# Kernel optimization log

Measured on AMD Instinct MI355X. Metric: run time of the kernel, lower is better.

## Reference

```python
import jax, jax.numpy as jnp
import numpy as np

EPS = 1e-6

def setup_inputs() -> dict:
    key = jax.random.key(0)
    M, N, D = 6, 4096, 512
    output = jax.random.normal(key, (M, N, D), dtype=jnp.float32)
    return {"output": output}

def reference(output):
    # output: [M, N, D] stacked per-layer features (already flatten(1)'d)
    M, N, _ = output.shape
    # Gram matrices K_i = X_i @ X_i^T with zeroed diagonal: [M, N, N]
    K = jnp.einsum('ind,imd->inm', output, output)
    K = K * (1.0 - jnp.eye(N, dtype=K.dtype))
    # Double centering H@K@H == K - rowmean - colmean + totalmean
    row = jnp.mean(K, axis=2, keepdims=True)
    col = jnp.mean(K, axis=1, keepdims=True)
    tot = jnp.mean(K, axis=(1, 2), keepdims=True)
    Khat = K - row - col + tot
    # Pairwise HSIC(K_i, K_j) = |sum(Khat_i * Khat_j)| : [M, M]
    S = jnp.abs(jnp.einsum('inm,jnm->ij', Khat, Khat))
    diag = jnp.diagonal(S)
    cka = S / jnp.sqrt(diag[:, None] * diag[None, :] + EPS)
    # Original only fills the strict lower triangle
    hsic_matrix = cka * jnp.tril(jnp.ones((M, M), dtype=cka.dtype), k=-1)
    l = jnp.sum(jnp.abs(hsic_matrix))
    hsic_visual = hsic_matrix + hsic_matrix.T + jnp.eye(M, dtype=cka.dtype)
    return (hsic_visual, l)
```

## Files before the change

### kernel.cpp

```cpp
#include <hip/hip_runtime.h>
#include <hip/hip_bf16.h>
#include <stdint.h>


#define NPTS  4096
#define DF    512
#define ML    6
#define NPAIR 21
#define BKB   128
#define KCHUNK_O 512
#define KCHUNK_D 1024
#define NDIAGBLK 240
#define NOFFBLK  960
#define NGEMMBLK (NDIAGBLK + NOFFBLK)

typedef float  f32x4 __attribute__((ext_vector_type(4)));
typedef unsigned char u8;
typedef long long i64;

__constant__ int c_PI[NPAIR] = {0,0,0,0,0,0, 1,1,1,1,1, 2,2,2,2, 3,3,3, 4,4, 5};
__constant__ int c_PJ[NPAIR] = {0,1,2,3,4,5, 1,2,3,4,5, 2,3,4,5, 3,4,5, 4,5, 5};
__constant__ int c_DIAGP[ML]  = {0, 6, 11, 15, 18, 20};
__constant__ int c_OFFP[15]   = {1,2,3,4,5, 7,8,9,10, 12,13,14, 16,17, 19};
__constant__ int c_TM[10] = {0,0,0,0, 1,1,1, 2,2, 3};
__constant__ int c_TN[10] = {0,1,2,3, 1,2,3, 2,3, 3};

#define OFF_XT8 0u
#define OFF_CP  12582912u
#define OFF_S   (OFF_CP + 15728640u)
#define OFF_F   (OFF_S + 12288u)
#define OFF_D   (OFF_F + 512u)
#define OFF_XS  (OFF_D + 98304u)
#define ZERO_BYTES (12288u + 512u + 98304u + 98304u)
#define OFF_DD  (OFF_XS + 98304u)
#define OFF_RD  (OFF_DD + 256u)
#define OFF_T   (OFF_RD + 256u)

__device__ __forceinline__ unsigned short f2fp8x2(float a, float b) {
    return (unsigned short)(__builtin_amdgcn_cvt_pk_fp8_f32(a, b, 0, false) & 0xffff);
}

__device__ __forceinline__ void gl2lds16(const void* g, void* l) {
    __builtin_amdgcn_global_load_lds(
        (__attribute__((address_space(1))) void*)g,
        (__attribute__((address_space(3))) void*)l, 16, 0, 0);
}

__global__ __launch_bounds__(256) void k_transpose(const float* __restrict__ X,
                                                   u8* __restrict__ Xt8,
                                                   float* __restrict__ s,
                                                   float* __restrict__ dv) {
    __shared__ float tT[64][67];
    int l = blockIdx.z, n0 = blockIdx.x * 64, d0 = blockIdx.y * 64;
    int t = threadIdx.x, q = t & 15, r = t >> 4;
    const float4* src = (const float4*)(X + ((size_t)l * NPTS + n0) * DF + d0);
#pragma unroll
    for (int p = 0; p < 4; ++p) {
        int rr = r + 16 * p;
        float4 v = src[(size_t)rr * (DF / 4) + q];
        tT[4 * q + 0][rr] = v.x;
        tT[4 * q + 1][rr] = v.y;
        tT[4 * q + 2][rr] = v.z;
        tT[4 * q + 3][rr] = v.w;
    }
    __syncthreads();
    if (t < 64) {
        float cs = 0.f;
#pragma unroll
        for (int k = 0; k < 64; ++k) {
            int n = (6 * t + k) & 63;
            cs += tT[t][n];
        }
        atomicAdd(&s[l * DF + d0 + t], cs);
    } else if (t < 128) {
        int n = t - 64;
        float rs = 0.f;
#pragma unroll
        for (int d = 0; d < 64; ++d) { float v = tT[d][n]; rs += v * v; }
        atomicAdd(&dv[l * NPTS + n0 + n], rs);
    }
    int dcol = t >> 2, nb = (t & 3) * 16;
    uint4 o;
#pragma unroll
    for (int w2 = 0; w2 < 4; ++w2) {
        int j = nb + w2 * 4;
        unsigned lo = f2fp8x2(tT[dcol][j + 0], tT[dcol][j + 1]);
        unsigned hi = f2fp8x2(tT[dcol][j + 2], tT[dcol][j + 3]);
        ((unsigned*)&o)[w2] = lo | (hi << 16);
    }
    *(uint4*)(Xt8 + ((size_t)(l * DF + d0 + dcol)) * NPTS + n0 + nb) = o;
}

__global__ __launch_bounds__(256) void k_rowdot(const u8* __restrict__ Xt8,
                                                const float* __restrict__ s,
                                                float* __restrict__ xs) {
    int l = blockIdx.z, d0 = blockIdx.y * 64, n0 = blockIdx.x * 1024;
    int t = threadIdx.x;
    __shared__ float sl[64];
    if (t < 64) sl[t] = s[l * DF + d0 + t];
    __syncthreads();
    const u8* base = Xt8 + ((size_t)(l * DF + d0)) * NPTS + n0 + t * 4;
    float a0 = 0, a1 = 0, a2 = 0, a3 = 0;
#pragma unroll 8
    for (int d = 0; d < 64; ++d) {
        unsigned v = *(const unsigned*)(base + (size_t)d * NPTS);
        float sv = sl[d];
        a0 += sv * __builtin_amdgcn_cvt_f32_fp8(v, 0);
        a1 += sv * __builtin_amdgcn_cvt_f32_fp8(v, 1);
        a2 += sv * __builtin_amdgcn_cvt_f32_fp8(v, 2);
        a3 += sv * __builtin_amdgcn_cvt_f32_fp8(v, 3);
    }
    float* o = xs + l * NPTS + n0 + t * 4;
    atomicAdd(&o[0], a0); atomicAdd(&o[1], a1);
    atomicAdd(&o[2], a2); atomicAdd(&o[3], a3);
}

__global__ __launch_bounds__(256) void k_pairdots(const float* __restrict__ dv,
                                                  const float* __restrict__ xs,
                                                  const float* __restrict__ s,
                                                  float* __restrict__ ddot,
                                                  float* __restrict__ rdot,
                                                  float* __restrict__ tb) {
    int p = blockIdx.x, i = c_PI[p], j = c_PJ[p];
    int t = threadIdx.x;
    const float invN = 1.0f / (float)NPTS;
    float dd = 0.f, rr = 0.f, sd = 0.f, ss = 0.f;
    for (int n = t; n < NPTS; n += 256) {
        float di = dv[i * NPTS + n], dj = dv[j * NPTS + n];
        float ri = (xs[i * NPTS + n] - di) * invN;
        float rj = (xs[j * NPTS + n] - dj) * invN;
        dd += di * dj;
        rr += ri * rj;
        sd += di;
    }
    for (int c = t; c < DF; c += 256) { float v = s[i * DF + c]; ss += v * v; }
    __shared__ float4 red[256];
    red[t] = make_float4(dd, rr, sd, ss);
    __syncthreads();
    for (int h = 128; h > 0; h >>= 1) {
        if (t < h) {
            float4 a = red[t], b = red[t + h];
            red[t] = make_float4(a.x + b.x, a.y + b.y, a.z + b.z, a.w + b.w);
        }
        __syncthreads();
    }
    if (t == 0) {
        ddot[p] = red[0].x;
        rdot[p] = red[0].y;
        if (i == j)
            tb[i] = (red[0].w - red[0].z) * (1.0f / ((float)NPTS * (float)NPTS));
    }
}

__global__ __launch_bounds__(256, 2) void k_gemm_frob(const u8* __restrict__ Xt8,
                                                      float* __restrict__ CP,
                                                      float* __restrict__ F) {
    __shared__ __align__(16) u8 As[128 * BKB];
    __shared__ __align__(16) u8 Bs[256 * BKB];

    int b = blockIdx.x;
    int t = threadIdx.x, wave = t >> 6, lane = t & 63;
    int rl = lane >> 3, g = lane & 7;
    int row16 = lane & 15, quad = lane >> 4;
    int qh = quad >> 1, qb = (quad & 1) * 8;

    if (b < NDIAGBLK) {
        int li = b / 40, rem = b % 40, tt = rem >> 2, z = rem & 3;
        int mt = c_TM[tt], nt = c_TN[tt];
        const u8* A = Xt8 + ((size_t)(li * DF + mt * 128)) * NPTS;
        const u8* B = Xt8 + ((size_t)(li * DF + nt * 128)) * NPTS;
        int kLo = z * KCHUNK_D, kHi = kLo + KCHUNK_D;

        int wr = (wave >> 1) * 64, wc = (wave & 1) * 64;
        f32x4 acc[4][4];
#pragma unroll
        for (int mi = 0; mi < 4; ++mi)
#pragma unroll
            for (int ni = 0; ni < 4; ++ni) acc[mi][ni] = (f32x4)0.0f;

        for (int k0 = kLo; k0 < kHi; k0 += BKB) {
            __syncthreads();
#pragma unroll
            for (int is = 0; is < 4; ++is) {
                int rbase = is * 32 + wave * 8;
                int r = rbase + rl;
                int gs = g ^ (r & 7);
                gl2lds16(A + (size_t)r * NPTS + k0 + gs * 16, &As[rbase * BKB]);
                gl2lds16(B + (size_t)r * NPTS + k0 + gs * 16, &Bs[rbase * BKB]);
            }
            __syncthreads();
#pragma unroll
            for (int ko = 0; ko < 4; ++ko) {
                int gi = ko * 2 + qh;
                i64 af[4], bf[4];
#pragma unroll
                for (int mi = 0; mi < 4; ++mi) {
                    int row = wr + mi * 16 + row16;
                    af[mi] = *(const i64*)&As[row * BKB + (gi ^ (row & 7)) * 16 + qb];
                }
#pragma unroll
                for (int ni = 0; ni < 4; ++ni) {
                    int row = wc + ni * 16 + row16;
                    bf[ni] = *(const i64*)&Bs[row * BKB + (gi ^ (row & 7)) * 16 + qb];
                }
#pragma unroll
                for (int mi = 0; mi < 4; ++mi)
#pragma unroll
                    for (int ni = 0; ni < 4; ++ni)
                        acc[mi][ni] = __builtin_amdgcn_mfma_f32_16x16x32_fp8_fp8(
                            af[mi], bf[ni], acc[mi][ni], 0, 0, 0);
            }
        }
        float* cp = CP + (((size_t)(li * 10 + tt) * 4 + z) * 16384) + wave * 4096;
#pragma unroll
        for (int mi = 0; mi < 4; ++mi)
#pragma unroll
            for (int ni = 0; ni < 4; ++ni)
#pragma unroll
                for (int e = 0; e < 4; ++e)
                    cp[(mi * 4 + ni) * 256 + e * 64 + lane] = acc[mi][ni][e];
    } else {
        int b2 = b - NDIAGBLK;
        int op = b2 >> 6, rem = b2 & 63;
        int tile = rem >> 3, z = rem & 7;
        int pp = c_OFFP[op];
        const u8* A = Xt8 + ((size_t)(c_PI[pp] * DF + (tile & 3) * 128)) * NPTS;
        const u8* B = Xt8 + ((size_t)(c_PJ[pp] * DF + (tile >> 2) * 256)) * NPTS;
        int kLo = z * KCHUNK_O, kHi = kLo + KCHUNK_O;

        int wr = (wave >> 1) * 64, wc = (wave & 1) * 128;
        f32x4 acc[4][8];
#pragma unroll
        for (int mi = 0; mi < 4; ++mi)
#pragma unroll
            for (int ni = 0; ni < 8; ++ni) acc[mi][ni] = (f32x4)0.0f;

        for (int k0 = kLo; k0 < kHi; k0 += BKB) {
            __syncthreads();
#pragma unroll
            for (int is = 0; is < 4; ++is) {
                int rbase = is * 32 + wave * 8;
                int r = rbase + rl;
                int gs = g ^ (r & 7);
                gl2lds16(A + (size_t)r * NPTS + k0 + gs * 16, &As[rbase * BKB]);
            }
#pragma unroll
            for (int is = 0; is < 8; ++is) {
                int rbase = is * 32 + wave * 8;
                int r = rbase + rl;
                int gs = g ^ (r & 7);
                gl2lds16(B + (size_t)r * NPTS + k0 + gs * 16, &Bs[rbase * BKB]);
            }
            __syncthreads();
#pragma unroll
            for (int ko = 0; ko < 4; ++ko) {
                int gi = ko * 2 + qh;
                i64 af[4], bf[8];
#pragma unroll
                for (int mi = 0; mi < 4; ++mi) {
                    int row = wr + mi * 16 + row16;
                    af[mi] = *(const i64*)&As[row * BKB + (gi ^ (row & 7)) * 16 + qb];
                }
#pragma unroll
                for (int ni = 0; ni < 8; ++ni) {
                    int row = wc + ni * 16 + row16;
                    bf[ni] = *(const i64*)&Bs[row * BKB + (gi ^ (row & 7)) * 16 + qb];
                }
#pragma unroll
                for (int mi = 0; mi < 4; ++mi)
#pragma unroll
                    for (int ni = 0; ni < 8; ++ni)
                        acc[mi][ni] = __builtin_amdgcn_mfma_f32_16x16x32_fp8_fp8(
                            af[mi], bf[ni], acc[mi][ni], 0, 0, 0);
            }
        }
        float local = 0.f;
#pragma unroll
        for (int mi = 0; mi < 4; ++mi)
#pragma unroll
            for (int ni = 0; ni < 8; ++ni)
#pragma unroll
                for (int e = 0; e < 4; ++e)
                    local += acc[mi][ni][e] * acc[mi][ni][e];
        for (int off = 32; off; off >>= 1) local += __shfl_down(local, off);
        __shared__ float wsum[4];
        if (lane == 0) wsum[wave] = local;
        __syncthreads();
        if (t == 0) atomicAdd(&F[pp], wsum[0] + wsum[1] + wsum[2] + wsum[3]);
    }
}

__global__ __launch_bounds__(256) void k_diagred(const float* __restrict__ CP,
                                                 float* __restrict__ F) {
    int b = blockIdx.x;
    int li = b / 10, tt = b % 10;
    int t = threadIdx.x;
    const float* base = CP + (size_t)b * 4 * 16384;
    float a = 0.f;
#pragma unroll 4
    for (int c = 0; c < 64; ++c) {
        int idx = c * 256 + t;
        float v = base[idx] + base[16384 + idx]
                + base[2 * 16384 + idx] + base[3 * 16384 + idx];
        a += v * v;
    }
    for (int off = 32; off; off >>= 1) a += __shfl_down(a, off);
    __shared__ float wsum[4];
    if ((t & 63) == 0) wsum[t >> 6] = a;
    __syncthreads();
    if (t == 0) {
        float w = (c_TM[tt] == c_TN[tt]) ? 1.0f : 2.0f;
        atomicAdd(&F[c_DIAGP[li]], w * (wsum[0] + wsum[1] + wsum[2] + wsum[3]));
    }
}

__global__ __launch_bounds__(64) void k_finalize(const float* __restrict__ F,
                                                 const float* __restrict__ ddot,
                                                 const float* __restrict__ rdot,
                                                 const float* __restrict__ tb,
                                                 float* __restrict__ out) {
    __shared__ double hs[ML][ML];
    __shared__ float cka[ML][ML];
    int t = threadIdx.x;
    if (t < NPAIR) {
        int i = c_PI[t], j = c_PJ[t];
        double v = (double)F[t] - (double)ddot[t]
                 - 2.0 * (double)NPTS * (double)rdot[t]
                 + (double)NPTS * (double)NPTS * (double)tb[i] * (double)tb[j];
        hs[i][j] = v; hs[j][i] = v;
    }
    __syncthreads();
    if (t < ML * ML) {
        int i = t / ML, j = t % ML;
        float v;
        if (i == j) v = 1.0f;
        else v = (float)(fabs(hs[i][j]) / sqrt(hs[i][i] * hs[j][j] + 1e-6));
        cka[i][j] = v;
        out[t] = v;
    }
    __syncthreads();
    if (t == 0) {
        float l = 0.f;
        for (int i = 1; i < ML; ++i)
            for (int j = 0; j < i; ++j) l += cka[i][j];
        out[ML * ML] = l;
    }
}

extern "C" void kernel_launch(void* const* d_in, const int* in_sizes, int n_in,
                              void* d_out, int out_size, void* d_ws, size_t ws_size,
                              hipStream_t stream) {
    (void)in_sizes; (void)n_in; (void)out_size; (void)ws_size;
    const float* X = (const float*)d_in[0];
    float* out = (float*)d_out;
    char* ws = (char*)d_ws;
    u8*    Xt8 = (u8*)(ws + OFF_XT8);
    float* CP  = (float*)(ws + OFF_CP);
    float* s   = (float*)(ws + OFF_S);
    float* F   = (float*)(ws + OFF_F);
    float* dv  = (float*)(ws + OFF_D);
    float* xs  = (float*)(ws + OFF_XS);
    float* dd  = (float*)(ws + OFF_DD);
    float* rd  = (float*)(ws + OFF_RD);
    float* tb  = (float*)(ws + OFF_T);

    hipMemsetAsync(ws + OFF_S, 0, ZERO_BYTES, stream);

    hipLaunchKernelGGL(k_transpose, dim3(64, 8, 6), dim3(256), 0, stream, X, Xt8, s, dv);
    hipLaunchKernelGGL(k_gemm_frob, dim3(NGEMMBLK), dim3(256), 0, stream, Xt8, CP, F);
    hipLaunchKernelGGL(k_diagred,   dim3(60),       dim3(256), 0, stream, CP, F);
    hipLaunchKernelGGL(k_rowdot,    dim3(4, 8, 6),  dim3(256), 0, stream, Xt8, s, xs);
    hipLaunchKernelGGL(k_pairdots,  dim3(NPAIR),    dim3(256), 0, stream, dv, xs, s, dd, rd, tb);
    hipLaunchKernelGGL(k_finalize,  dim3(1),        dim3(64),  0, stream, F, dd, rd, tb, out);
}
```

Before: 145.5 us.

## Fuse stats into GEMM grid and merge tail kernels, drop memset and atomics

Replaces the memset and global atomics in the transpose with per-tile partial sums, which a few extra blocks appended to the GEMM launch then reduce. Those blocks also compute the row-dot term that k_rowdot used to handle. The diagonal reduction, pair dots and finalize are merged into one tail kernel that uses a last-block counter. This cuts six launches plus a memset down to three, at the cost of extra partial-sum traffic and slow serial stats blocks in the GEMM grid.

Result: slower. 167.6 us (+15.2%).

```diff
diff --git a/kernel.cpp b/kernel.cpp
--- a/kernel.cpp
+++ b/kernel.cpp
@@ -13,6 +13,8 @@
 #define NDIAGBLK 240
 #define NOFFBLK  960
 #define NGEMMBLK (NDIAGBLK + NOFFBLK)
+#define NSTATS   24
+#define NTAIL    81
 
 typedef float  f32x4 __attribute__((ext_vector_type(4)));
 typedef unsigned char u8;
@@ -27,14 +29,15 @@
 
 #define OFF_XT8 0u
 #define OFF_CP  12582912u
-#define OFF_S   (OFF_CP + 15728640u)
-#define OFF_F   (OFF_S + 12288u)
-#define OFF_D   (OFF_F + 512u)
-#define OFF_XS  (OFF_D + 98304u)
-#define ZERO_BYTES (12288u + 512u + 98304u + 98304u)
-#define OFF_DD  (OFF_XS + 98304u)
-#define OFF_RD  (OFF_DD + 256u)
-#define OFF_T   (OFF_RD + 256u)
+#define OFF_SP  28311552u
+#define OFF_DVP 29097984u
+#define OFF_S   29884416u
+#define OFF_F   29896704u
+#define OFF_D   29897216u
+#define OFF_XS  29995520u
+#define OFF_DD  30093824u
+#define OFF_RD  30094080u
+#define OFF_T   30094336u
 
 __device__ __forceinline__ unsigned short f2fp8x2(float a, float b) {
     return (unsigned short)(__builtin_amdgcn_cvt_pk_fp8_f32(a, b, 0, false) & 0xffff);
@@ -48,11 +51,18 @@
 
 __global__ __launch_bounds__(256) void k_transpose(const float* __restrict__ X,
                                                    u8* __restrict__ Xt8,
-                                                   float* __restrict__ s,
-                                                   float* __restrict__ dv) {
+                                                   float* __restrict__ sp,
+                                                   float* __restrict__ dvp,
+                                                   float* __restrict__ F,
+                                                   unsigned* __restrict__ cnt) {
     __shared__ float tT[64][67];
-    int l = blockIdx.z, n0 = blockIdx.x * 64, d0 = blockIdx.y * 64;
+    int nt = blockIdx.x, dt = blockIdx.y, l = blockIdx.z;
+    int n0 = nt * 64, d0 = dt * 64;
     int t = threadIdx.x, q = t & 15, r = t >> 4;
+    if (nt == 0 && dt == 0 && l == 0) {
+        if (t >= 128 && t < 128 + NPAIR) F[t - 128] = 0.f;
+        if (t == 155) *cnt = 0u;
+    }
     const float4* src = (const float4*)(X + ((size_t)l * NPTS + n0) * DF + d0);
 #pragma unroll
     for (int p = 0; p < 4; ++p) {
@@ -71,13 +81,13 @@
             int n = (6 * t + k) & 63;
             cs += tT[t][n];
         }
-        atomicAdd(&s[l * DF + d0 + t], cs);
+        sp[((l << 6) + nt) * DF + d0 + t] = cs;
     } else if (t < 128) {
         int n = t - 64;
         float rs = 0.f;
 #pragma unroll
         for (int d = 0; d < 64; ++d) { float v = tT[d][n]; rs += v * v; }
-        atomicAdd(&dv[l * NPTS + n0 + n], rs);
+        dvp[((l << 3) + dt) * NPTS + n0 + n] = rs;
     }
     int dcol = t >> 2, nb = (t & 3) * 16;
     uint4 o;
@@ -91,70 +101,14 @@
     *(uint4*)(Xt8 + ((size_t)(l * DF + d0 + dcol)) * NPTS + n0 + nb) = o;
 }
 
-__global__ __launch_bounds__(256) void k_rowdot(const u8* __restrict__ Xt8,
-                                                const float* __restrict__ s,
-                                                float* __restrict__ xs) {
-    int l = blockIdx.z, d0 = blockIdx.y * 64, n0 = blockIdx.x * 1024;
-    int t = threadIdx.x;
-    __shared__ float sl[64];
-    if (t < 64) sl[t] = s[l * DF + d0 + t];
-    __syncthreads();
-    const u8* base = Xt8 + ((size_t)(l * DF + d0)) * NPTS + n0 + t * 4;
-    float a0 = 0, a1 = 0, a2 = 0, a3 = 0;
-#pragma unroll 8
-    for (int d = 0; d < 64; ++d) {
-        unsigned v = *(const unsigned*)(base + (size_t)d * NPTS);
-        float sv = sl[d];
-        a0 += sv * __builtin_amdgcn_cvt_f32_fp8(v, 0);
-        a1 += sv * __builtin_amdgcn_cvt_f32_fp8(v, 1);
-        a2 += sv * __builtin_amdgcn_cvt_f32_fp8(v, 2);
-        a3 += sv * __builtin_amdgcn_cvt_f32_fp8(v, 3);
-    }
-    float* o = xs + l * NPTS + n0 + t * 4;
-    atomicAdd(&o[0], a0); atomicAdd(&o[1], a1);
-    atomicAdd(&o[2], a2); atomicAdd(&o[3], a3);
-}
-
-__global__ __launch_bounds__(256) void k_pairdots(const float* __restrict__ dv,
-                                                  const float* __restrict__ xs,
-                                                  const float* __restrict__ s,
-                                                  float* __restrict__ ddot,
-                                                  float* __restrict__ rdot,
-                                                  float* __restrict__ tb) {
-    int p = blockIdx.x, i = c_PI[p], j = c_PJ[p];
-    int t = threadIdx.x;
-    const float invN = 1.0f / (float)NPTS;
-    float dd = 0.f, rr = 0.f, sd = 0.f, ss = 0.f;
-    for (int n = t; n < NPTS; n += 256) {
-        float di = dv[i * NPTS + n], dj = dv[j * NPTS + n];
-        float ri = (xs[i * NPTS + n] - di) * invN;
-        float rj = (xs[j * NPTS + n] - dj) * invN;
-        dd += di * dj;
-        rr += ri * rj;
-        sd += di;
-    }
-    for (int c = t; c < DF; c += 256) { float v = s[i * DF + c]; ss += v * v; }
-    __shared__ float4 red[256];
-    red[t] = make_float4(dd, rr, sd, ss);
-    __syncthreads();
-    for (int h = 128; h > 0; h >>= 1) {
-        if (t < h) {
-            float4 a = red[t], b = red[t + h];
-            red[t] = make_float4(a.x + b.x, a.y + b.y, a.z + b.z, a.w + b.w);
-        }
-        __syncthreads();
-    }
-    if (t == 0) {
-        ddot[p] = red[0].x;
-        rdot[p] = red[0].y;
-        if (i == j)
-            tb[i] = (red[0].w - red[0].z) * (1.0f / ((float)NPTS * (float)NPTS));
-    }
-}
-
 __global__ __launch_bounds__(256, 2) void k_gemm_frob(const u8* __restrict__ Xt8,
                                                       float* __restrict__ CP,
-                                                      float* __restrict__ F) {
+                                                      float* __restrict__ F,
+                                                      const float* __restrict__ sp,
+                                                      const float* __restrict__ dvp,
+                                                      float* __restrict__ s,
+                                                      float* __restrict__ dv,
+                                                      float* __restrict__ xs) {
     __shared__ __align__(16) u8 As[128 * BKB];
     __shared__ __align__(16) u8 Bs[256 * BKB];
 
@@ -219,7 +173,7 @@
 #pragma unroll
                 for (int e = 0; e < 4; ++e)
                     cp[(mi * 4 + ni) * 256 + e * 64 + lane] = acc[mi][ni][e];
-    } else {
+    } else if (b < NGEMMBLK) {
         int b2 = b - NDIAGBLK;
         int op = b2 >> 6, rem = b2 & 63;
         int tile = rem >> 3, z = rem & 7;
@@ -287,46 +241,130 @@
         if (lane == 0) wsum[wave] = local;
         __syncthreads();
         if (t == 0) atomicAdd(&F[pp], wsum[0] + wsum[1] + wsum[2] + wsum[3]);
-    }
-}
-
-__global__ __launch_bounds__(256) void k_diagred(const float* __restrict__ CP,
-                                                 float* __restrict__ F) {
-    int b = blockIdx.x;
-    int li = b / 10, tt = b % 10;
-    int t = threadIdx.x;
-    const float* base = CP + (size_t)b * 4 * 16384;
-    float a = 0.f;
-#pragma unroll 4
-    for (int c = 0; c < 64; ++c) {
-        int idx = c * 256 + t;
-        float v = base[idx] + base[16384 + idx]
-                + base[2 * 16384 + idx] + base[3 * 16384 + idx];
-        a += v * v;
-    }
-    for (int off = 32; off; off >>= 1) a += __shfl_down(a, off);
+    } else {
+        int sid = b - NGEMMBLK;
+        int l = sid >> 2, nc = sid & 3;
+        int n0 = nc * 1024;
+        float* sl = (float*)As;
+        for (int d = t; d < DF; d += 256) {
+            float a = 0.f;
+#pragma unroll 8
+            for (int nt = 0; nt < 64; ++nt) a += sp[((l << 6) + nt) * DF + d];
+            sl[d] = a;
+            if (nc == 0) s[l * DF + d] = a;
+        }
+        __syncthreads();
+        const u8* xb = Xt8 + (size_t)l * DF * NPTS + n0 + t * 4;
+        float a0 = 0, a1 = 0, a2 = 0, a3 = 0;
+#pragma unroll 8
+        for (int d = 0; d < DF; ++d) {
+            unsigned v = *(const unsigned*)(xb + (size_t)d * NPTS);
+            float sv = sl[d];
+            a0 += sv * __builtin_amdgcn_cvt_f32_fp8(v, 0);
+            a1 += sv * __builtin_amdgcn_cvt_f32_fp8(v, 1);
+            a2 += sv * __builtin_amdgcn_cvt_f32_fp8(v, 2);
+            a3 += sv * __builtin_amdgcn_cvt_f32_fp8(v, 3);
+        }
+        int n = n0 + t * 4;
+        float* xo = xs + l * NPTS + n;
+        xo[0] = a0; xo[1] = a1; xo[2] = a2; xo[3] = a3;
+#pragma unroll
+        for (int j = 0; j < 4; ++j) {
+            float dsum = 0.f;
+#pragma unroll
+            for (int dt2 = 0; dt2 < 8; ++dt2)
+                dsum += dvp[((l << 3) + dt2) * NPTS + n + j];
+            dv[l * NPTS + n + j] = dsum;
+        }
+    }
+}
+
+__global__ __launch_bounds__(256) void k_tail(const float* __restrict__ CP,
+                                              const float* __restrict__ dv,
+                                              const float* __restrict__ xs,
+                                              const float* __restrict__ s,
+                                              float* __restrict__ F,
+                                              float* __restrict__ ddot,
+                                              float* __restrict__ rdot,
+                                              float* __restrict__ tb,
+                                              unsigned* __restrict__ cnt,
+                                              float* __restrict__ out) {
     __shared__ float wsum[4];
-    if ((t & 63) == 0) wsum[t >> 6] = a;
-    __syncthreads();
-    if (t == 0) {
-        float w = (c_TM[tt] == c_TN[tt]) ? 1.0f : 2.0f;
-        atomicAdd(&F[c_DIAGP[li]], w * (wsum[0] + wsum[1] + wsum[2] + wsum[3]));
-    }
-}
-
-__global__ __launch_bounds__(64) void k_finalize(const float* __restrict__ F,
-                                                 const float* __restrict__ ddot,
-                                                 const float* __restrict__ rdot,
-                                                 const float* __restrict__ tb,
-                                                 float* __restrict__ out) {
+    __shared__ float4 red[256];
+    __shared__ int lastFlag;
+    __shared__ float tbv[ML];
     __shared__ double hs[ML][ML];
     __shared__ float cka[ML][ML];
-    int t = threadIdx.x;
+
+    int b = blockIdx.x, t = threadIdx.x;
+
+    if (b < 60) {
+        int li = b / 10, tt = b % 10;
+        const float* base = CP + (size_t)b * 4 * 16384;
+        float a = 0.f;
+#pragma unroll 4
+        for (int c = 0; c < 64; ++c) {
+            int idx = c * 256 + t;
+            float v = base[idx] + base[16384 + idx]
+                    + base[2 * 16384 + idx] + base[3 * 16384 + idx];
+            a += v * v;
+        }
+        for (int off = 32; off; off >>= 1) a += __shfl_down(a, off);
+        if ((t & 63) == 0) wsum[t >> 6] = a;
+        __syncthreads();
+        if (t == 0) {
+            float w = (c_TM[tt] == c_TN[tt]) ? 1.0f : 2.0f;
+            atomicAdd(&F[c_DIAGP[li]], w * (wsum[0] + wsum[1] + wsum[2] + wsum[3]));
+        }
+    } else {
+        int p = b - 60, i = c_PI[p], j = c_PJ[p];
+        const float invN = 1.0f / (float)NPTS;
+        float dd = 0.f, rr = 0.f, sd = 0.f, ss = 0.f;
+        for (int n = t; n < NPTS; n += 256) {
+            float di = dv[i * NPTS + n], dj = dv[j * NPTS + n];
+            float ri = (xs[i * NPTS + n] - di) * invN;
+            float rj = (xs[j * NPTS + n] - dj) * invN;
+            dd += di * dj;
+            rr += ri * rj;
+            sd += di;
+        }
+        for (int c = t; c < DF; c += 256) { float v = s[i * DF + c]; ss += v * v; }
+        red[t] = make_float4(dd, rr, sd, ss);
+        __syncthreads();
+        for (int h = 128; h > 0; h >>= 1) {
+            if (t < h) {
+                float4 a = red[t], bb = red[t + h];
+                red[t] = make_float4(a.x + bb.x, a.y + bb.y, a.z + bb.z, a.w + bb.w);
+            }
+            __syncthreads();
+        }
+        if (t == 0) {
+            atomicExch(&ddot[p], red[0].x);
+            atomicExch(&rdot[p], red[0].y);
+            if (i == j)
+                atomicExch(&tb[i],
+                    (red[0].w - red[0].z) * (1.0f / ((float)NPTS * (float)NPTS)));
+        }
+    }
+
+    __syncthreads();
+    if (t == 0) {
+        __threadfence();
+        unsigned old = atomicAdd(cnt, 1u);
+        lastFlag = (old == NTAIL - 1);
+    }
+    __syncthreads();
+    if (!lastFlag) return;
+    __threadfence();
+    if (t < ML) tbv[t] = atomicAdd(&tb[t], 0.0f);
+    __syncthreads();
     if (t < NPAIR) {
         int i = c_PI[t], j = c_PJ[t];
-        double v = (double)F[t] - (double)ddot[t]
-                 - 2.0 * (double)NPTS * (double)rdot[t]
-                 + (double)NPTS * (double)NPTS * (double)tb[i] * (double)tb[j];
+        double Fv = (double)atomicAdd(&F[t], 0.0f);
+        double dd = (double)atomicAdd(&ddot[t], 0.0f);
+        double rd = (double)atomicAdd(&rdot[t], 0.0f);
+        double v = Fv - dd - 2.0 * (double)NPTS * rd
+                 + (double)NPTS * (double)NPTS * (double)tbv[i] * (double)tbv[j];
         hs[i][j] = v; hs[j][i] = v;
     }
     __syncthreads();
@@ -356,20 +394,21 @@
     char* ws = (char*)d_ws;
     u8*    Xt8 = (u8*)(ws + OFF_XT8);
     float* CP  = (float*)(ws + OFF_CP);
+    float* sp  = (float*)(ws + OFF_SP);
+    float* dvp = (float*)(ws + OFF_DVP);
     float* s   = (float*)(ws + OFF_S);
     float* F   = (float*)(ws + OFF_F);
+    unsigned* cnt = (unsigned*)(ws + OFF_F + 256u);
     float* dv  = (float*)(ws + OFF_D);
     float* xs  = (float*)(ws + OFF_XS);
     float* dd  = (float*)(ws + OFF_DD);
     float* rd  = (float*)(ws + OFF_RD);
     float* tb  = (float*)(ws + OFF_T);
 
-    hipMemsetAsync(ws + OFF_S, 0, ZERO_BYTES, stream);
-
-    hipLaunchKernelGGL(k_transpose, dim3(64, 8, 6), dim3(256), 0, stream, X, Xt8, s, dv);
-    hipLaunchKernelGGL(k_gemm_frob, dim3(NGEMMBLK), dim3(256), 0, stream, Xt8, CP, F);
-    hipLaunchKernelGGL(k_diagred,   dim3(60),       dim3(256), 0, stream, CP, F);
-    hipLaunchKernelGGL(k_rowdot,    dim3(4, 8, 6),  dim3(256), 0, stream, Xt8, s, xs);
-    hipLaunchKernelGGL(k_pairdots,  dim3(NPAIR),    dim3(256), 0, stream, dv, xs, s, dd, rd, tb);
-    hipLaunchKernelGGL(k_finalize,  dim3(1),        dim3(64),  0, stream, F, dd, rd, tb, out);
-}
+    hipLaunchKernelGGL(k_transpose, dim3(64, 8, 6), dim3(256), 0, stream,
+                       X, Xt8, sp, dvp, F, cnt);
+    hipLaunchKernelGGL(k_gemm_frob, dim3(NGEMMBLK + NSTATS), dim3(256), 0, stream,
+                       Xt8, CP, F, sp, dvp, s, dv, xs);
+    hipLaunchKernelGGL(k_tail, dim3(NTAIL), dim3(256), 0, stream,
+                       CP, dv, xs, s, F, dd, rd, tb, cnt, out);
+}
```
